# Performance work log

Measured on AMD Instinct MI355X. Metric: run time of the kernel, lower is better.

The kernel has to match this reference:

```python
import jax, jax.numpy as jnp
import numpy as np
from jax import lax
import math

KS = 7  # attention kernel size
PAD = 3


def conv2d(x, w, b, pad):
    y = lax.conv_general_dilated(x, w, (1, 1), [(pad, pad), (pad, pad)],
                                 dimension_numbers=('NCHW', 'OIHW', 'NCHW'))
    return y + b[None, :, None, None]


def unfold(x):
    # x: [B, C, H, W] -> [B, C, KS*KS, H, W], matching nn.Unfold channel-major order
    B, C, H, W = x.shape
    xp = jnp.pad(x, ((0, 0), (0, 0), (PAD, PAD), (PAD, PAD)))
    patches = [xp[:, :, i:i + H, j:j + W] for i in range(KS) for j in range(KS)]
    return jnp.stack(patches, axis=2)


def setup_inputs() -> dict:
    key = jax.random.key(0)
    ks = jax.random.split(key, 12)
    B, H, W = 1, 256, 256
    s = lambda fan: 1.0 / np.sqrt(fan)
    inp = {
        'x': jax.random.normal(ks[0], (B, 6, H, W), jnp.float32),
        'w0': jax.random.normal(ks[1], (48, 3, 3, 3), jnp.float32) * s(3 * 9),
        'b0': jnp.zeros((48,), jnp.float32),
        'w1': jax.random.normal(ks[2], (48, 48, 3, 3), jnp.float32) * s(48 * 9),
        'b1': jnp.zeros((48,), jnp.float32),
        'w2': jax.random.normal(ks[3], (48, 48, 3, 3), jnp.float32) * s(48 * 9),
        'b2': jnp.zeros((48,), jnp.float32),
        'w3': jax.random.normal(ks[4], (24, 48, 3, 3), jnp.float32) * s(48 * 9),
        'b3': jnp.zeros((24,), jnp.float32),
        'skip_w': jax.random.normal(ks[5], (24, 3, 1, 1), jnp.float32) * s(3),
        'skip_b': jnp.zeros((24,), jnp.float32),
        'q_w': jax.random.normal(ks[6], (24, 24, 1, 1), jnp.float32) * s(24),
        'q_b': jnp.zeros((24,), jnp.float32),
        'k_w': jax.random.normal(ks[7], (24, 24, 1, 1), jnp.float32) * s(24),
        'k_b': jnp.zeros((24,), jnp.float32),
        'v_w': jax.random.normal(ks[8], (24, 24, 1, 1), jnp.float32) * s(24),
        'v_b': jnp.zeros((24,), jnp.float32),
    }
    return inp


def reference(x, w0, b0, w1, b1, w2, b2, w3, b3, skip_w, skip_b,
              q_w, q_b, k_w, k_b, v_w, v_b):
    def submodel(t):
        h = jax.nn.relu(conv2d(t, w0, b0, 1))
        h = jax.nn.relu(conv2d(h, w1, b1, 1))
        h = jax.nn.relu(conv2d(h, w2, b2, 1))
        h = jax.nn.relu(conv2d(h, w3, b3, 1))
        return h + conv2d(t, skip_w, skip_b, 0)

    xa, xb = jnp.split(x, 2, axis=1)  # [B,3,H,W] each
    a = submodel(xa)                  # [B,24,H,W]
    b = submodel(xb)

    Q = conv2d(b, q_w, q_b, 0)        # [B,24,H,W]
    K = unfold(conv2d(a, k_w, k_b, 0))  # [B,24,49,H,W]
    V = unfold(conv2d(a, v_w, v_b, 0))  # [B,24,49,H,W]

    C = Q.shape[1]
    A = jnp.einsum('bchw,bcphw->bphw', Q, K) / math.sqrt(C)
    A = jax.nn.softmax(A, axis=1)     # softmax over 49 local positions
    y = jnp.einsum('bphw,bcphw->bchw', A, V)
    return jnp.concatenate([y + a, b], axis=1)  # [B,48,H,W]
```

## Files before the change

kernel.cpp:

```cpp
#include <hip/hip_runtime.h>
#include <math.h>

#define HH 256
#define WW 256
#define NN (HH * WW)

typedef _Float16 f16;
typedef _Float16 f16x4 __attribute__((ext_vector_type(4)));
typedef _Float16 f16x8 __attribute__((ext_vector_type(8)));
typedef float f32x4 __attribute__((ext_vector_type(4)));

#define OQ 75264
#define CS 56
#define IS 40

__device__ inline float dot8p(f16x8 a, f16x8 b, float acc) {
#if __has_builtin(__builtin_amdgcn_fdot2)
  acc = __builtin_amdgcn_fdot2(__builtin_shufflevector(a, a, 0, 1),
                               __builtin_shufflevector(b, b, 0, 1), acc, false);
  acc = __builtin_amdgcn_fdot2(__builtin_shufflevector(a, a, 2, 3),
                               __builtin_shufflevector(b, b, 2, 3), acc, false);
  acc = __builtin_amdgcn_fdot2(__builtin_shufflevector(a, a, 4, 5),
                               __builtin_shufflevector(b, b, 4, 5), acc, false);
  acc = __builtin_amdgcn_fdot2(__builtin_shufflevector(a, a, 6, 7),
                               __builtin_shufflevector(b, b, 6, 7), acc, false);
  return acc;
#else
#pragma unroll
  for (int i = 0; i < 8; ++i) acc += (float)a[i] * (float)b[i];
  return acc;
#endif
}

__device__ __forceinline__ float repack_elem(
    int e, const float* __restrict__ w0, const float* __restrict__ w1,
    const float* __restrict__ w2, const float* __restrict__ w3,
    const float* __restrict__ qw, const float* __restrict__ kw,
    const float* __restrict__ vw) {
  const int O1 = 1536, O2 = O1 + 27648, O3 = O2 + 27648;
  float val = 0.f;
  if (e >= OQ) {
    int idx = e - OQ;
    int mat = idx >> 10;
    int r = idx & 1023;
    int nt = r >> 9;
    int ln = (r >> 3) & 63;
    int j = r & 7;
    int nn = ln & 15, qd = ln >> 4;
    int ci = qd * 8 + j, co = nt * 16 + nn;
    const float* w = (mat == 0) ? qw : (mat == 1) ? kw : vw;
    if (ci < 24 && co < 24) val = w[co * 24 + ci];
  } else if (e < O1) {
    int j = e & 7;
    int ln = (e >> 3) & 63;
    int nt = e >> 9;
    int nn = ln & 15, qd = ln >> 4;
    int k = qd * 8 + j;
    int cout = nt * 16 + nn;
    if (k < 27) {
      int tap = k / 3, ci = k - tap * 3;
      val = w0[(cout * 3 + ci) * 9 + tap];
    }
  } else {
    const float* w;
    int COUT, idx;
    if (e < O2)      { w = w1; COUT = 48; idx = e - O1; }
    else if (e < O3) { w = w2; COUT = 48; idx = e - O2; }
    else             { w = w3; COUT = 24; idx = e - O3; }
    const int NT = (COUT == 48) ? 3 : 2;
    int j = idx & 7;
    int ln = (idx >> 3) & 63;
    int rest = idx >> 9;
    int nt = rest % NT;
    int q2 = rest / NT;
    int kc = q2 & 1;
    int tap = q2 >> 1;
    int nn = ln & 15, qd = ln >> 4;
    int ci = kc * 32 + qd * 8 + j;
    int cout = nt * 16 + nn;
    if (ci < 48 && cout < COUT) val = w[(cout * 48 + ci) * 9 + tap];
  }
  return val;
}

__global__ __launch_bounds__(256) void prep(
    const float* __restrict__ w0, const float* __restrict__ w1,
    const float* __restrict__ w2, const float* __restrict__ w3,
    const float* __restrict__ qw, const float* __restrict__ kw,
    const float* __restrict__ vw, f16* __restrict__ bf) {
  int e = blockIdx.x * 256 + threadIdx.x;
  bf[e] = (f16)repack_elem(e, w0, w1, w2, w3, qw, kw, vw);
}

template <int W_IN, int W_OUT, int H_OUT, int MAXT>
__device__ __forceinline__ void stage_mid(const f16* __restrict__ inb,
                                          f16* __restrict__ outb,
                                          const f16* __restrict__ bfr,
                                          const float* __restrict__ bias,
                                          int gy0, int gx0, int tid) {
  const int P = W_OUT * H_OUT;
  const int T = (P + 15) >> 4;
  const int lane = tid & 63, wave = tid >> 6;
  const int n = lane & 15, quad = lane >> 4;
  const int cbase = quad * 4;
  f32x4 acc[MAXT][3];
  int ay[MAXT], ax[MAXT];
  float4 bv[3];
#pragma unroll
  for (int nt = 0; nt < 3; ++nt)
    bv[nt] = *(const float4*)(bias + nt * 16 + cbase);
#pragma unroll
  for (int ti = 0; ti < MAXT; ++ti) {
    int qa = (wave + 4 * ti) * 16 + n;
    int qc = (qa > P - 1) ? (P - 1) : qa;
    ay[ti] = qc / W_OUT;
    ax[ti] = qc - ay[ti] * W_OUT;
#pragma unroll
    for (int nt = 0; nt < 3; ++nt)
      acc[ti][nt] = (f32x4){bv[nt].x, bv[nt].y, bv[nt].z, bv[nt].w};
  }
#pragma unroll 1
  for (int tap = 0; tap < 9; ++tap) {
    const int dy = tap / 3, dx = tap - dy * 3;
    f16x8 B[2][3];
#pragma unroll
    for (int kc = 0; kc < 2; ++kc)
#pragma unroll
      for (int nt = 0; nt < 3; ++nt)
        B[kc][nt] =
            *(const f16x8*)(bfr + (((tap * 2 + kc) * 3 + nt) * 64 + lane) * 8);
#pragma unroll
    for (int ti = 0; ti < MAXT; ++ti) {
      if (wave + 4 * ti < T) {
        const f16* ap = inb + ((ay[ti] + dy) * W_IN + ax[ti] + dx) * CS +
                        quad * 8;
        f16x8 a0 = *(const f16x8*)(ap);
        f16x8 a1 = *(const f16x8*)(ap + 32);
#pragma unroll
        for (int nt = 0; nt < 3; ++nt)
          acc[ti][nt] = __builtin_amdgcn_mfma_f32_16x16x32_f16(
              B[0][nt], a0, acc[ti][nt], 0, 0, 0);
#pragma unroll
        for (int nt = 0; nt < 3; ++nt)
          acc[ti][nt] = __builtin_amdgcn_mfma_f32_16x16x32_f16(
              B[1][nt], a1, acc[ti][nt], 0, 0, 0);
      }
    }
  }
#pragma unroll
  for (int ti = 0; ti < MAXT; ++ti) {
    int qa = (wave + 4 * ti) * 16 + n;
    if (wave + 4 * ti < T && qa < P) {
      int gy = gy0 + ay[ti], gx = gx0 + ax[ti];
      bool im = (gy >= 0 && gy < HH && gx >= 0 && gx < WW);
#pragma unroll
      for (int nt = 0; nt < 3; ++nt) {
        f16x4 h;
#pragma unroll
        for (int reg = 0; reg < 4; ++reg)
          h[reg] = (f16)(im ? fmaxf(acc[ti][nt][reg], 0.f) : 0.f);
        *(f16x4*)(outb + qa * CS + nt * 16 + cbase) = h;
      }
    }
  }
}

__global__ __launch_bounds__(256, 2) void fused_conv(
    const float* __restrict__ x, const float* __restrict__ b0,
    const float* __restrict__ b1, const float* __restrict__ b2,
    const float* __restrict__ b3, const float* __restrict__ sw,
    const float* __restrict__ sb, f16* __restrict__ ABh,
    const f16* __restrict__ BF) {
  extern __shared__ char smem[];
  f16* bufA = (f16*)smem;
  f16* bufB = (f16*)(smem + 34496);
  const int tid = threadIdx.x;
  const int bz = blockIdx.x;
  const int z = bz >> 9, tt = bz & 511;
  const int bx = (tt & 15) * 16, by = (tt >> 4) * 8;
  const int lane = tid & 63, wave = tid >> 6;
  const int n = lane & 15, quad = lane >> 4;
  const int cbase = quad * 4;
  const float* xz = x + (size_t)z * 3 * NN;

  f16x8 B0[3];
#pragma unroll
  for (int nt = 0; nt < 3; ++nt)
    B0[nt] = *(const f16x8*)(BF + (nt * 64 + lane) * 8);

  for (int i = tid; i < 3840; i += 256) {
    f16x8 zz = {};
    *(f16x8*)(smem + i * 16) = zz;
  }
  __syncthreads();

  for (int p = tid; p < 308; p += 256) {
    int py = p / 22, px = p - py * 22;
    int gy = by - 3 + py, gx = bx - 3 + px;
    f16 row[32];
#pragma unroll
    for (int k = 27; k < 32; ++k) row[k] = (f16)0.f;
#pragma unroll
    for (int tap = 0; tap < 9; ++tap) {
      int dy = tap / 3, dx = tap - (tap / 3) * 3;
      int sy = gy + dy - 1, sx = gx + dx - 1;
      f16 c0 = (f16)0.f, c1 = c0, c2 = c0;
      if (sy >= 0 && sy < HH && sx >= 0 && sx < WW) {
        int o = sy * WW + sx;
        c0 = (f16)xz[o];
        c1 = (f16)xz[NN + o];
        c2 = (f16)xz[2 * NN + o];
      }
      row[tap * 3 + 0] = c0;
      row[tap * 3 + 1] = c1;
      row[tap * 3 + 2] = c2;
    }
    f16* dst = bufB + p * IS;
#pragma unroll
    for (int c = 0; c < 4; ++c)
      *(f16x8*)(dst + c * 8) = *(f16x8*)(row + c * 8);
  }
  __syncthreads();

  {
    float4 bv[3];
#pragma unroll
    for (int nt = 0; nt < 3; ++nt)
      bv[nt] = *(const float4*)(b0 + nt * 16 + cbase);
    f32x4 acc[5][3];
    int pya[5], pxa[5];
#pragma unroll
    for (int ti = 0; ti < 5; ++ti) {
      int qa = (wave + 4 * ti) * 16 + n;
      int qc = (qa > 307) ? 307 : qa;
      pya[ti] = qc / 22;
      pxa[ti] = qc - pya[ti] * 22;
#pragma unroll
      for (int nt = 0; nt < 3; ++nt)
        acc[ti][nt] = (f32x4){bv[nt].x, bv[nt].y, bv[nt].z, bv[nt].w};
    }
#pragma unroll
    for (int ti = 0; ti < 5; ++ti) {
      int qa = (wave + 4 * ti) * 16 + n;
      int qc = (qa > 307) ? 307 : qa;
      f16x8 a = *(const f16x8*)(bufB + qc * IS + quad * 8);
#pragma unroll
      for (int nt = 0; nt < 3; ++nt)
        acc[ti][nt] = __builtin_amdgcn_mfma_f32_16x16x32_f16(B0[nt], a,
                                                             acc[ti][nt], 0,
                                                             0, 0);
    }
    __syncthreads();
#pragma unroll
    for (int ti = 0; ti < 5; ++ti) {
      int qa = (wave + 4 * ti) * 16 + n;
      if (qa < 308) {
        int gy = by - 3 + pya[ti], gx = bx - 3 + pxa[ti];
        bool im = (gy >= 0 && gy < HH && gx >= 0 && gx < WW);
#pragma unroll
        for (int nt = 0; nt < 3; ++nt) {
          f16x4 h;
#pragma unroll
          for (int reg = 0; reg < 4; ++reg)
            h[reg] = (f16)(im ? fmaxf(acc[ti][nt][reg], 0.f) : 0.f);
          *(f16x4*)(bufA + qa * CS + nt * 16 + cbase) = h;
        }
      }
    }
  }
  __syncthreads();

  stage_mid<22, 20, 12, 4>(bufA, bufB, BF + 1536, b1, by - 2, bx - 2, tid);
  __syncthreads();
  stage_mid<20, 18, 10, 3>(bufB, bufA, BF + 29184, b2, by - 1, bx - 1, tid);
  __syncthreads();

  {
    f32x4 acc[2][2];
    int ay[2], ax[2];
    float skw0[2][4], skw1[2][4], skw2[2][4], skb4[2][4];
#pragma unroll
    for (int nt = 0; nt < 2; ++nt)
#pragma unroll
      for (int reg = 0; reg < 4; ++reg) {
        int cc = nt * 16 + cbase + reg;
        bool v = (cc < 24);
        skw0[nt][reg] = v ? sw[cc * 3 + 0] : 0.f;
        skw1[nt][reg] = v ? sw[cc * 3 + 1] : 0.f;
        skw2[nt][reg] = v ? sw[cc * 3 + 2] : 0.f;
        skb4[nt][reg] = v ? sb[cc] : 0.f;
      }
#pragma unroll
    for (int ti = 0; ti < 2; ++ti) {
      int qa = (wave + 4 * ti) * 16 + n;
      ay[ti] = qa >> 4;
      ax[ti] = qa & 15;
#pragma unroll
      for (int nt = 0; nt < 2; ++nt) {
        int cc0 = nt * 16 + cbase;
        float4 bv = (cc0 < 24) ? *(const float4*)(b3 + cc0)
                               : make_float4(0.f, 0.f, 0.f, 0.f);
        acc[ti][nt] = (f32x4){bv.x, bv.y, bv.z, bv.w};
      }
    }
#pragma unroll 1
    for (int tap = 0; tap < 9; ++tap) {
      const int dy = tap / 3, dx = tap - dy * 3;
      f16x8 B[2][2];
#pragma unroll
      for (int kc = 0; kc < 2; ++kc)
#pragma unroll
        for (int nt = 0; nt < 2; ++nt)
          B[kc][nt] = *(const f16x8*)(BF + 56832 +
                                      (((tap * 2 + kc) * 2 + nt) * 64 + lane) *
                                          8);
#pragma unroll
      for (int ti = 0; ti < 2; ++ti) {
        const f16* ap = bufA + ((ay[ti] + dy) * 18 + ax[ti] + dx) * CS +
                        quad * 8;
        f16x8 a0 = *(const f16x8*)(ap);
        f16x8 a1 = *(const f16x8*)(ap + 32);
#pragma unroll
        for (int nt = 0; nt < 2; ++nt)
          acc[ti][nt] = __builtin_amdgcn_mfma_f32_16x16x32_f16(
              B[0][nt], a0, acc[ti][nt], 0, 0, 0);
#pragma unroll
        for (int nt = 0; nt < 2; ++nt)
          acc[ti][nt] = __builtin_amdgcn_mfma_f32_16x16x32_f16(
              B[1][nt], a1, acc[ti][nt], 0, 0, 0);
      }
    }
    f16* oz = ABh + (size_t)z * NN * 32;
#pragma unroll
    for (int ti = 0; ti < 2; ++ti) {
      int o = (by + ay[ti]) * WW + bx + ax[ti];
      float xv0 = xz[o], xv1 = xz[NN + o], xv2 = xz[2 * NN + o];
#pragma unroll
      for (int nt = 0; nt < 2; ++nt) {
        int cc0 = nt * 16 + cbase;
        if (cc0 < 24) {
          f16x4 h;
#pragma unroll
          for (int reg = 0; reg < 4; ++reg) {
            float sk = skb4[nt][reg] + skw0[nt][reg] * xv0 +
                       skw1[nt][reg] * xv1 + skw2[nt][reg] * xv2;
            h[reg] = (f16)(fmaxf(acc[ti][nt][reg], 0.f) + sk);
          }
          *(f16x4*)(oz + (size_t)o * 32 + cc0) = h;
        }
      }
    }
#pragma unroll
    for (int ti = 0; ti < 2; ++ti) {
      int o = (by + ay[ti]) * WW + bx + ax[ti];
      if (quad >= 2) {
        f16x4 zz = {};
        *(f16x4*)(oz + (size_t)o * 32 + 16 + cbase) = zz;
      }
    }
  }
}

__global__ __launch_bounds__(256, 3) void attn_q(
    const f16* __restrict__ ABh, const f16* __restrict__ BF,
    const float* __restrict__ qw, const float* __restrict__ qb,
    const float* __restrict__ kb, const float* __restrict__ vb,
    float* __restrict__ out) {
  extern __shared__ char smem[];
  f16* kv = (f16*)smem;
  f16* Wq = (f16*)(smem + 35840);
  float* Qbv = (float*)(smem + 35840 + 1152);
  const int tid = threadIdx.x;
  const int lane = tid & 63, wave = tid >> 6;
  const int n = lane & 15, quad = lane >> 4;
  const int cbase = quad * 4;
  const int bxA = ((int)blockIdx.x & 15) * 16, byA = ((int)blockIdx.x >> 4) * 8;

  for (int i = tid; i < 576; i += 256) Wq[i] = (f16)qw[i];
  if (tid < 24) Qbv[tid] = qb[tid];

  for (int idx = tid; idx < 1232; idx += 256) {
    int slot = idx >> 2, c = idx & 3;
    int row = slot / 22, pxl = slot - row * 22;
    int gy = byA + row - 3, gx = bxA + pxl - 3;
    f16x8 v = {};
    if (gy >= 0 && gy < HH && gx >= 0 && gx < WW)
      v = *(const f16x8*)(ABh + ((size_t)(gy * WW + gx)) * 32 + c * 8);
    *(f16x8*)(kv + slot * 56 + c * 8) = v;
  }
  __syncthreads();

  const int t7 = tid & 127, half = tid >> 7;
  const int yl = t7 >> 4, xl = t7 & 15;
  const int pg = (byA + yl) * WW + bxA + xl;

  const f16* cs = kv + ((yl + 3) * 22 + (xl + 3)) * 56;
  f16x8 a0 = *(const f16x8*)(cs);
  f16x8 a1 = *(const f16x8*)(cs + 8);
  f16x8 a2 = *(const f16x8*)(cs + 16);

  const f16* bhp = ABh + (size_t)NN * 32 + (size_t)pg * 32;
  f16x8 bb0 = *(const f16x8*)(bhp);
  f16x8 bb1 = *(const f16x8*)(bhp + 8);
  f16x8 bb2 = *(const f16x8*)(bhp + 16);
  float qf[24];
#pragma unroll
  for (int co = 0; co < 24; ++co) {
    float acc = Qbv[co];
    acc = dot8p(bb0, *(const f16x8*)(Wq + co * 24), acc);
    acc = dot8p(bb1, *(const f16x8*)(Wq + co * 24 + 8), acc);
    acc = dot8p(bb2, *(const f16x8*)(Wq + co * 24 + 16), acc);
    qf[co] = acc;
  }
  f16x8 q0, q1, q2;
#pragma unroll
  for (int c = 0; c < 8; ++c) {
    q0[c] = (f16)qf[c];
    q1[c] = (f16)qf[8 + c];
    q2[c] = (f16)qf[16 + c];
  }
  __syncthreads();

  {
    f16x8 KF[2], VF[2];
#pragma unroll
    for (int nt = 0; nt < 2; ++nt) {
      KF[nt] = *(const f16x8*)(BF + OQ + 1024 + (nt * 64 + lane) * 8);
      VF[nt] = *(const f16x8*)(BF + OQ + 2048 + (nt * 64 + lane) * 8);
    }
    float4 kb4[2], vb4[2];
#pragma unroll
    for (int nt = 0; nt < 2; ++nt) {
      int cc0 = nt * 16 + cbase;
      kb4[nt] = (cc0 < 24) ? *(const float4*)(kb + cc0)
                           : make_float4(0.f, 0.f, 0.f, 0.f);
      vb4[nt] = (cc0 < 24) ? *(const float4*)(vb + cc0)
                           : make_float4(0.f, 0.f, 0.f, 0.f);
    }
    for (int t = wave; t < 20; t += 4) {
      f16x8 a8 = *(const f16x8*)(kv + (t * 16 + n) * 56 + quad * 8);
      f16x4 hk[2], hv[2];
#pragma unroll
      for (int nt = 0; nt < 2; ++nt) {
        f32x4 ak = {kb4[nt].x, kb4[nt].y, kb4[nt].z, kb4[nt].w};
        f32x4 av = {vb4[nt].x, vb4[nt].y, vb4[nt].z, vb4[nt].w};
        ak = __builtin_amdgcn_mfma_f32_16x16x32_f16(KF[nt], a8, ak, 0, 0, 0);
        av = __builtin_amdgcn_mfma_f32_16x16x32_f16(VF[nt], a8, av, 0, 0, 0);
#pragma unroll
        for (int reg = 0; reg < 4; ++reg) {
          hk[nt][reg] = (f16)ak[reg];
          hv[nt][reg] = (f16)av[reg];
        }
      }
      f16* slot = kv + (t * 16 + n) * 56;
#pragma unroll
      for (int nt = 0; nt < 2; ++nt) {
        int cc0 = nt * 16 + cbase;
        if (cc0 < 24) {
          *(f16x4*)(slot + cc0) = hk[nt];
          *(f16x4*)(slot + 24 + cc0) = hv[nt];
        }
      }
    }
  }
  __syncthreads();

  float s[25];
  float m = -3e38f;
#pragma unroll
  for (int i = 0; i < 25; ++i) {
    int pp = half * 25 + i;
    if (pp < 49) {
      int dy = pp / 7, dx = pp - (pp / 7) * 7;
      const f16* base = kv + ((yl + dy) * 22 + (xl + dx)) * 56;
      f16x8 k0 = *(const f16x8*)(base);
      f16x8 k1 = *(const f16x8*)(base + 8);
      f16x8 k2 = *(const f16x8*)(base + 16);
      float d = 0.f;
      d = dot8p(q0, k0, d);
      d = dot8p(q1, k1, d);
      d = dot8p(q2, k2, d);
      s[i] = d * 0.20412414523193154f;
      m = fmaxf(m, s[i]);
    } else {
      s[i] = -3e38f;
    }
  }
  float den = 0.f;
#pragma unroll
  for (int i = 0; i < 25; ++i) {
    float e = __expf(s[i] - m);
    s[i] = e;
    den += e;
  }

  f16x8 y0 = {}, y1 = {}, y2 = {};
#pragma unroll
  for (int i = 0; i < 25; ++i) {
    int pp = half * 25 + i;
    if (pp < 49) {
      int dy = pp / 7, dx = pp - (pp / 7) * 7;
      const f16* base = kv + ((yl + dy) * 22 + (xl + dx)) * 56 + 24;
      f16 wh = (f16)s[i];
      f16x8 w8 = {wh, wh, wh, wh, wh, wh, wh, wh};
      f16x8 v0 = *(const f16x8*)(base);
      f16x8 v1 = *(const f16x8*)(base + 8);
      f16x8 v2 = *(const f16x8*)(base + 16);
      y0 = v0 * w8 + y0;
      y1 = v1 * w8 + y1;
      y2 = v2 * w8 + y2;
    }
  }
  __syncthreads();

  if (half == 1) {
    f16* ex = kv + t7 * 56;
    *(f16x8*)(ex) = y0;
    *(f16x8*)(ex + 8) = y1;
    *(f16x8*)(ex + 16) = y2;
    float* mf = (float*)(ex + 24);
    mf[0] = m;
    mf[1] = den;
  }
  __syncthreads();

  if (half == 0) {
    const f16* ex = kv + t7 * 56;
    f16x8 yb0 = *(const f16x8*)(ex);
    f16x8 yb1 = *(const f16x8*)(ex + 8);
    f16x8 yb2 = *(const f16x8*)(ex + 16);
    const float* mf = (const float*)(ex + 24);
    float mB = mf[0], dB = mf[1];
    float M = fmaxf(m, mB);
    float fa = __expf(m - M), fb = __expf(mB - M);
    float inv = 1.f / (den * fa + dB * fb);
#pragma unroll
    for (int c = 0; c < 8; ++c) {
      out[(size_t)c * NN + pg] =
          ((float)y0[c] * fa + (float)yb0[c] * fb) * inv + (float)a0[c];
      out[(size_t)(8 + c) * NN + pg] =
          ((float)y1[c] * fa + (float)yb1[c] * fb) * inv + (float)a1[c];
      out[(size_t)(16 + c) * NN + pg] =
          ((float)y2[c] * fa + (float)yb2[c] * fb) * inv + (float)a2[c];
    }
  } else {
#pragma unroll
    for (int c = 0; c < 8; ++c) {
      out[(size_t)(24 + c) * NN + pg] = (float)bb0[c];
      out[(size_t)(32 + c) * NN + pg] = (float)bb1[c];
      out[(size_t)(40 + c) * NN + pg] = (float)bb2[c];
    }
  }
}

extern "C" void kernel_launch(void* const* d_in, const int* in_sizes, int n_in,
                              void* d_out, int out_size, void* d_ws,
                              size_t ws_size, hipStream_t stream) {
  const float* x = (const float*)d_in[0];
  const float* w0 = (const float*)d_in[1];
  const float* b0 = (const float*)d_in[2];
  const float* w1 = (const float*)d_in[3];
  const float* b1 = (const float*)d_in[4];
  const float* w2 = (const float*)d_in[5];
  const float* b2 = (const float*)d_in[6];
  const float* w3 = (const float*)d_in[7];
  const float* b3 = (const float*)d_in[8];
  const float* sw = (const float*)d_in[9];
  const float* sb = (const float*)d_in[10];
  const float* qw = (const float*)d_in[11];
  const float* qb = (const float*)d_in[12];
  const float* kw = (const float*)d_in[13];
  const float* kb = (const float*)d_in[14];
  const float* vw = (const float*)d_in[15];
  const float* vb = (const float*)d_in[16];
  float* out = (float*)d_out;

  f16* base = (f16*)d_ws;
  f16* ABh = base;
  f16* BF = base + (size_t)64 * NN;

  prep<<<dim3(306), dim3(256), 0, stream>>>(w0, w1, w2, w3, qw, kw, vw, BF);
  fused_conv<<<dim3(1024), dim3(256), 61440, stream>>>(x, b0, b1, b2, b3, sw,
                                                       sb, ABh, BF);
  attn_q<<<dim3(512), dim3(256), 37088, stream>>>(ABh, BF, qw, qb, kb, vb,
                                                  out);
}
```

Before: 151.2 us.

## Shrink attention tile to 8x8 pixels and split 49 taps across four waves

The attention kernel now processes an 8x8 pixel tile per block (1024 blocks) instead of 16x8, and each pixel's 49 neighbourhood taps are split four ways across the block's waves instead of two, with a four-way online-softmax merge through shared memory. Shared memory drops, launch bounds rise to four blocks per CU, and per-thread register arrays shrink, all aimed at more occupancy and parallelism. In exchange, the halo overhead grows (14x14 loads per 64 pixels versus 22x14 per 128), the K/V projection recomputes more halo pixels, and there is an extra merge step with more synchronisation traffic.

```diff
diff --git a/kernel.cpp b/kernel.cpp
--- a/kernel.cpp
+++ b/kernel.cpp
@@ -361,27 +361,27 @@
   }
 }
 
-__global__ __launch_bounds__(256, 3) void attn_q(
+__global__ __launch_bounds__(256, 4) void attn_q(
     const f16* __restrict__ ABh, const f16* __restrict__ BF,
     const float* __restrict__ qw, const float* __restrict__ qb,
     const float* __restrict__ kb, const float* __restrict__ vb,
     float* __restrict__ out) {
   extern __shared__ char smem[];
   f16* kv = (f16*)smem;
-  f16* Wq = (f16*)(smem + 35840);
-  float* Qbv = (float*)(smem + 35840 + 1152);
+  f16* Wq = (f16*)(smem + 21952);
+  float* Qbv = (float*)(smem + 21952 + 1152);
   const int tid = threadIdx.x;
   const int lane = tid & 63, wave = tid >> 6;
   const int n = lane & 15, quad = lane >> 4;
   const int cbase = quad * 4;
-  const int bxA = ((int)blockIdx.x & 15) * 16, byA = ((int)blockIdx.x >> 4) * 8;
+  const int bxA = ((int)blockIdx.x & 31) * 8, byA = ((int)blockIdx.x >> 5) * 8;
 
   for (int i = tid; i < 576; i += 256) Wq[i] = (f16)qw[i];
   if (tid < 24) Qbv[tid] = qb[tid];
 
-  for (int idx = tid; idx < 1232; idx += 256) {
+  for (int idx = tid; idx < 784; idx += 256) {
     int slot = idx >> 2, c = idx & 3;
-    int row = slot / 22, pxl = slot - row * 22;
+    int row = slot / 14, pxl = slot - row * 14;
     int gy = byA + row - 3, gx = bxA + pxl - 3;
     f16x8 v = {};
     if (gy >= 0 && gy < HH && gx >= 0 && gx < WW)
@@ -390,11 +390,11 @@
   }
   __syncthreads();
 
-  const int t7 = tid & 127, half = tid >> 7;
-  const int yl = t7 >> 4, xl = t7 & 15;
+  const int px = tid & 63, h = tid >> 6;
+  const int yl = px >> 3, xl = px & 7;
   const int pg = (byA + yl) * WW + bxA + xl;
 
-  const f16* cs = kv + ((yl + 3) * 22 + (xl + 3)) * 56;
+  const f16* cs = kv + ((yl + 3) * 14 + (xl + 3)) * 56;
   f16x8 a0 = *(const f16x8*)(cs);
   f16x8 a1 = *(const f16x8*)(cs + 8);
   f16x8 a2 = *(const f16x8*)(cs + 16);
@@ -437,8 +437,10 @@
       vb4[nt] = (cc0 < 24) ? *(const float4*)(vb + cc0)
                            : make_float4(0.f, 0.f, 0.f, 0.f);
     }
-    for (int t = wave; t < 20; t += 4) {
-      f16x8 a8 = *(const f16x8*)(kv + (t * 16 + n) * 56 + quad * 8);
+    for (int t = wave; t < 13; t += 4) {
+      int qa = t * 16 + n;
+      int qc = (qa > 195) ? 195 : qa;
+      f16x8 a8 = *(const f16x8*)(kv + qc * 56 + quad * 8);
       f16x4 hk[2], hv[2];
 #pragma unroll
       for (int nt = 0; nt < 2; ++nt) {
@@ -452,27 +454,29 @@
           hv[nt][reg] = (f16)av[reg];
         }
       }
-      f16* slot = kv + (t * 16 + n) * 56;
-#pragma unroll
-      for (int nt = 0; nt < 2; ++nt) {
-        int cc0 = nt * 16 + cbase;
-        if (cc0 < 24) {
-          *(f16x4*)(slot + cc0) = hk[nt];
-          *(f16x4*)(slot + 24 + cc0) = hv[nt];
+      if (qa < 196) {
+        f16* slot = kv + qa * 56;
+#pragma unroll
+        for (int nt = 0; nt < 2; ++nt) {
+          int cc0 = nt * 16 + cbase;
+          if (cc0 < 24) {
+            *(f16x4*)(slot + cc0) = hk[nt];
+            *(f16x4*)(slot + 24 + cc0) = hv[nt];
+          }
         }
       }
     }
   }
   __syncthreads();
 
-  float s[25];
+  float s[13];
   float m = -3e38f;
 #pragma unroll
-  for (int i = 0; i < 25; ++i) {
-    int pp = half * 25 + i;
+  for (int i = 0; i < 13; ++i) {
+    int pp = h * 13 + i;
     if (pp < 49) {
       int dy = pp / 7, dx = pp - (pp / 7) * 7;
-      const f16* base = kv + ((yl + dy) * 22 + (xl + dx)) * 56;
+      const f16* base = kv + ((yl + dy) * 14 + (xl + dx)) * 56;
       f16x8 k0 = *(const f16x8*)(base);
       f16x8 k1 = *(const f16x8*)(base + 8);
       f16x8 k2 = *(const f16x8*)(base + 16);
@@ -488,7 +492,7 @@
   }
   float den = 0.f;
 #pragma unroll
-  for (int i = 0; i < 25; ++i) {
+  for (int i = 0; i < 13; ++i) {
     float e = __expf(s[i] - m);
     s[i] = e;
     den += e;
@@ -496,11 +500,11 @@
 
   f16x8 y0 = {}, y1 = {}, y2 = {};
 #pragma unroll
-  for (int i = 0; i < 25; ++i) {
-    int pp = half * 25 + i;
+  for (int i = 0; i < 13; ++i) {
+    int pp = h * 13 + i;
     if (pp < 49) {
       int dy = pp / 7, dx = pp - (pp / 7) * 7;
-      const f16* base = kv + ((yl + dy) * 22 + (xl + dx)) * 56 + 24;
+      const f16* base = kv + ((yl + dy) * 14 + (xl + dx)) * 56 + 24;
       f16 wh = (f16)s[i];
       f16x8 w8 = {wh, wh, wh, wh, wh, wh, wh, wh};
       f16x8 v0 = *(const f16x8*)(base);
@@ -513,8 +517,8 @@
   }
   __syncthreads();
 
-  if (half == 1) {
-    f16* ex = kv + t7 * 56;
+  if (h != 0) {
+    f16* ex = kv + tid * 32;
     *(f16x8*)(ex) = y0;
     *(f16x8*)(ex + 8) = y1;
     *(f16x8*)(ex + 16) = y2;
@@ -524,26 +528,46 @@
   }
   __syncthreads();
 
-  if (half == 0) {
-    const f16* ex = kv + t7 * 56;
-    f16x8 yb0 = *(const f16x8*)(ex);
-    f16x8 yb1 = *(const f16x8*)(ex + 8);
-    f16x8 yb2 = *(const f16x8*)(ex + 16);
-    const float* mf = (const float*)(ex + 24);
-    float mB = mf[0], dB = mf[1];
-    float M = fmaxf(m, mB);
-    float fa = __expf(m - M), fb = __expf(mB - M);
-    float inv = 1.f / (den * fa + dB * fb);
+  if (h == 0) {
+    f16x8 p0[3], p1[3], p2[3];
+    float mm[3], dd[3];
+    float M = m;
+#pragma unroll
+    for (int hh = 0; hh < 3; ++hh) {
+      const f16* ex = kv + ((hh + 1) * 64 + px) * 32;
+      p0[hh] = *(const f16x8*)(ex);
+      p1[hh] = *(const f16x8*)(ex + 8);
+      p2[hh] = *(const f16x8*)(ex + 16);
+      const float* mf = (const float*)(ex + 24);
+      mm[hh] = mf[0];
+      dd[hh] = mf[1];
+      M = fmaxf(M, mm[hh]);
+    }
+    float f0 = __expf(m - M);
+    float fh[3];
+    float dtot = den * f0;
+#pragma unroll
+    for (int hh = 0; hh < 3; ++hh) {
+      fh[hh] = __expf(mm[hh] - M);
+      dtot += dd[hh] * fh[hh];
+    }
+    const float inv = 1.f / dtot;
 #pragma unroll
     for (int c = 0; c < 8; ++c) {
-      out[(size_t)c * NN + pg] =
-          ((float)y0[c] * fa + (float)yb0[c] * fb) * inv + (float)a0[c];
-      out[(size_t)(8 + c) * NN + pg] =
-          ((float)y1[c] * fa + (float)yb1[c] * fb) * inv + (float)a1[c];
-      out[(size_t)(16 + c) * NN + pg] =
-          ((float)y2[c] * fa + (float)yb2[c] * fb) * inv + (float)a2[c];
-    }
-  } else {
+      float v0 = (float)y0[c] * f0;
+      float v1 = (float)y1[c] * f0;
+      float v2 = (float)y2[c] * f0;
+#pragma unroll
+      for (int hh = 0; hh < 3; ++hh) {
+        v0 += (float)p0[hh][c] * fh[hh];
+        v1 += (float)p1[hh][c] * fh[hh];
+        v2 += (float)p2[hh][c] * fh[hh];
+      }
+      out[(size_t)c * NN + pg] = v0 * inv + (float)a0[c];
+      out[(size_t)(8 + c) * NN + pg] = v1 * inv + (float)a1[c];
+      out[(size_t)(16 + c) * NN + pg] = v2 * inv + (float)a2[c];
+    }
+  } else if (h == 1) {
 #pragma unroll
     for (int c = 0; c < 8; ++c) {
       out[(size_t)(24 + c) * NN + pg] = (float)bb0[c];
@@ -582,6 +606,6 @@
   prep<<<dim3(306), dim3(256), 0, stream>>>(w0, w1, w2, w3, qw, kw, vw, BF);
   fused_conv<<<dim3(1024), dim3(256), 61440, stream>>>(x, b0, b1, b2, b3, sw,
                                                        sb, ABh, BF);
-  attn_q<<<dim3(512), dim3(256), 37088, stream>>>(ABh, BF, qw, qb, kb, vb,
-                                                  out);
+  attn_q<<<dim3(1024), dim3(256), 23200, stream>>>(ABh, BF, qw, qb, kb, vb,
+                                                   out);
 }
```

New measurement: 167.2 us. 10.6% more time.
